# Optimization experiments

Hardware: AMD Instinct MI355X
Metric: run time of the kernel (lower is better)

Reference implementation:

```python
import jax, jax.numpy as jnp
import numpy as np


def _dct_ortho(x):
    # DCT-II with 'ortho' norm over the last axis, matching the torch impl.
    N = x.shape[-1]
    v = jnp.concatenate([x[..., ::2], x[..., 1::2][..., ::-1]], axis=-1)
    Vc = jnp.fft.fft(v, axis=-1)
    k = -jnp.arange(N, dtype=x.dtype) * (np.pi / (2 * N))
    V = Vc.real * jnp.cos(k) - Vc.imag * jnp.sin(k)
    scale = jnp.concatenate([
        jnp.full((1,), np.sqrt(N) * 2, dtype=x.dtype),
        jnp.full((N - 1,), np.sqrt(N / 2) * 2, dtype=x.dtype)])
    return 2 * (V / scale)


def _idct_ortho(X):
    # Inverse of _dct_ortho (DCT-III, 'ortho') over the last axis.
    N = X.shape[-1]
    Xv = X / 2
    scale = jnp.concatenate([
        jnp.full((1,), np.sqrt(N) * 2, dtype=X.dtype),
        jnp.full((N - 1,), np.sqrt(N / 2) * 2, dtype=X.dtype)])
    Xv = Xv * scale
    k = jnp.arange(N, dtype=X.dtype) * (np.pi / (2 * N))
    Wr, Wi = jnp.cos(k), jnp.sin(k)
    Vti = jnp.concatenate([jnp.zeros_like(Xv[..., :1]), -Xv[..., ::-1][..., :-1]], axis=-1)
    Vr = Xv * Wr - Vti * Wi
    Vi = Xv * Wi + Vti * Wr
    Vc = jax.lax.complex(Vr, Vi)
    # torch.fft.irfft(V, n=N) uses only the first N//2+1 complex entries.
    v = jnp.fft.irfft(Vc[..., : N // 2 + 1], n=N, axis=-1)
    out = jnp.zeros_like(v)
    out = out.at[..., ::2].set(v[..., : N - N // 2])
    out = out.at[..., 1::2].set(v[..., ::-1][..., : N // 2])
    return out


def _spectral_mix(xc, w):
    # xc: (B, I, A, B2, S) channel-first; w: (I, O, modes)
    modes = w.shape[-1]
    xf = _dct_ortho(xc)
    out = jnp.einsum('bixyz,ioz->boxyz', xf[..., :modes], w)
    out = jnp.pad(out, [(0, 0)] * 4 + [(0, xc.shape[-1] - modes)])
    return _idct_ortho(out)


def setup_inputs() -> dict:
    key = jax.random.key(0)
    ks = jax.random.split(key, 8)
    B, S, I, O, M = 4, 64, 32, 32, 16
    factor = 2
    x = jax.random.normal(ks[0], (B, S, S, S, I), dtype=jnp.float32)
    # xavier_normal_ for (in, out, modes): fan_in = out*modes, fan_out = in*modes
    std = float(np.sqrt(2.0 / (O * M + I * M)))
    fw_x = jax.random.normal(ks[1], (I, O, M), dtype=jnp.float32) * std
    fw_y = jax.random.normal(ks[2], (I, O, M), dtype=jnp.float32) * std
    fw_z = jax.random.normal(ks[3], (I, O, M), dtype=jnp.float32) * std
    # 2-layer backcast FF: Linear(O, O*factor) + ReLU, Linear(O*factor, O)
    lim0 = float(1.0 / np.sqrt(O))
    lim1 = float(1.0 / np.sqrt(O * factor))
    w0 = jax.random.uniform(ks[4], (O, O * factor), jnp.float32, -lim0, lim0)
    b0 = jax.random.uniform(ks[5], (O * factor,), jnp.float32, -lim0, lim0)
    w1 = jax.random.uniform(ks[6], (O * factor, O), jnp.float32, -lim1, lim1)
    b1 = jax.random.uniform(ks[7], (O,), jnp.float32, -lim1, lim1)
    return {"x": x, "fw_x": fw_x, "fw_y": fw_y, "fw_z": fw_z,
            "w0": w0, "b0": b0, "w1": w1, "b1": b1}


def reference(x, fw_x, fw_y, fw_z, w0, b0, w1, b1):
    # (B, S1, S2, S3, I) -> (B, I, S1, S2, S3)
    xc = jnp.transpose(x, (0, 4, 1, 2, 3))
    # z-axis (last dim already)
    xz = _spectral_mix(xc, fw_z)
    # y-axis
    xy = jnp.swapaxes(_spectral_mix(jnp.swapaxes(xc, -1, -2), fw_y), -1, -2)
    # x-axis
    xx = jnp.swapaxes(_spectral_mix(jnp.swapaxes(xc, -1, -3), fw_x), -1, -3)
    h = xx + xy + xz
    h = jnp.transpose(h, (0, 2, 3, 4, 1))  # back to channels-last
    # backcast FeedForward (dropout=0, eval): Linear -> ReLU -> Linear
    h = jax.nn.relu(h @ w0 + b0)
    b_out = h @ w1 + b1
    return b_out
```

## Files before the change

### kernel.cpp

```cpp
#include <hip/hip_runtime.h>
#include <math.h>

using f4 = __attribute__((ext_vector_type(4))) float;

#define NS 64
#define NI 32
#define NK 16

#define OFF_D   0
#define OFF_WTZ 1024
#define OFF_WTY (1024 + 16384)
#define OFF_WTX (1024 + 2*16384)
#define OFF_W0T (1024 + 3*16384)
#define WS_FLOATS (1024 + 3*16384 + 2048)

__device__ inline float dot4(f4 a, f4 b) { f4 p = a * b; return p[0] + p[1] + p[2] + p[3]; }

__global__ __launch_bounds__(256) void init_kernel(
    const float* __restrict__ fw_x, const float* __restrict__ fw_y,
    const float* __restrict__ fw_z, const float* __restrict__ w0,
    float* __restrict__ ws)
{
    int gid = blockIdx.x * 256 + threadIdx.x;
    if (gid < 1024) {
        int k = gid >> 6, n = gid & 63;
        float s = (k == 0) ? 0.125f : sqrtf(2.0f / 64.0f);
        ws[OFF_D + gid] = s * cospif((float)((2 * n + 1) * k) / 128.0f);
    } else if (gid < 1024 + 3 * 16384) {
        int r = gid - 1024;
        int a = r / 16384;
        int q = r % 16384;
        int k = q >> 10;
        int i = (q >> 5) & 31;
        int o = q & 31;
        const float* fw = (a == 0) ? fw_z : (a == 1) ? fw_y : fw_x;
        ws[1024 + a * 16384 + q] = fw[(i * 32 + o) * 16 + k];
    } else if (gid < WS_FLOATS) {
        int r = gid - (1024 + 3 * 16384);
        int j = r >> 5, i = r & 31;
        ws[OFF_W0T + r] = w0[i * 64 + j];
    }
}

template<int AXIS, int MODE>
__global__ __launch_bounds__(256) void axis_kernel(
    const float* __restrict__ x, float* __restrict__ h,
    const float* __restrict__ ws, const float* __restrict__ w1g,
    const float* __restrict__ b0g, const float* __restrict__ b1g)
{
    __shared__ f4 Xl[2048];
    __shared__ f4 Ul[512];
    __shared__ f4 Vl[512];
    __shared__ float Dl[1024];

    const int t = threadIdx.x;
    const int bid = blockIdx.x;
    const int b  = bid >> 10;
    const int c1 = (bid >> 4) & 63;
    const int c2 = bid & 15;

    const float* Dg = ws + OFF_D;
    const float* Wt = ws + (AXIS == 2 ? OFF_WTZ : AXIS == 1 ? OFF_WTY : OFF_WTX);

    int base, strideM, strideS;
    if (AXIS == 2) { base = ((b * 64 + c1) * 64 + c2 * 4) * 2048;      strideM = 32;     strideS = 2048; }
    if (AXIS == 1) { base = (b * 64 + c1) * 131072 + c2 * 128;         strideM = 2048;   strideS = 32; }
    if (AXIS == 0) { base = b * 8388608 + c1 * 2048 + c2 * 128;        strideM = 131072; strideS = 32; }

    #pragma unroll
    for (int q = 0; q < 4; ++q) Dl[t + 256 * q] = Dg[t + 256 * q];

    const f4* xg = reinterpret_cast<const f4*>(x);
    if (AXIS == 2) {
        int b4 = base >> 2;
        #pragma unroll
        for (int q = 0; q < 8; ++q) Xl[t + 256 * q] = xg[b4 + t + 256 * q];
    } else {
        #pragma unroll
        for (int q = 0; q < 8; ++q) {
            int j = t + 256 * q;
            int m = j >> 5, c = j & 31;
            Xl[j] = xg[((base + m * strideM) >> 2) + c];
        }
    }
    __syncthreads();

    #pragma unroll
    for (int it = 0; it < 2; ++it) {
        int id = t + 256 * it;
        int i4 = id & 7, k = (id >> 3) & 15, s = id >> 7;
        f4 acc = {0.f, 0.f, 0.f, 0.f};
        #pragma unroll
        for (int m = 0; m < 64; ++m) {
            f4 xv = Xl[AXIS == 2 ? (s * 512 + m * 8 + i4) : (m * 32 + s * 8 + i4)];
            acc += xv * Dl[k * 64 + m];
        }
        Ul[s * 128 + k * 8 + i4] = acc;
    }
    __syncthreads();

    if (t < 128) {
        int k = t >> 3, o4 = t & 7;
        const f4* Wt4 = reinterpret_cast<const f4*>(Wt);
        const float* Us = reinterpret_cast<const float*>(Ul);
        f4 v0 = {0.f,0.f,0.f,0.f}, v1 = v0, v2 = v0, v3 = v0;
        #pragma unroll 8
        for (int i = 0; i < 32; ++i) {
            f4 w = Wt4[k * 256 + i * 8 + o4];
            v0 += w * Us[0 * 512 + k * 32 + i];
            v1 += w * Us[1 * 512 + k * 32 + i];
            v2 += w * Us[2 * 512 + k * 32 + i];
            v3 += w * Us[3 * 512 + k * 32 + i];
        }
        Vl[0 * 128 + k * 8 + o4] = v0;
        Vl[1 * 128 + k * 8 + o4] = v1;
        Vl[2 * 128 + k * 8 + o4] = v2;
        Vl[3 * 128 + k * 8 + o4] = v3;
    }
    __syncthreads();

    f4* hg = reinterpret_cast<f4*>(h);
    #pragma unroll
    for (int it = 0; it < 8; ++it) {
        int id = t + 256 * it;
        int o4 = id & 7, n = (id >> 3) & 63, s = id >> 9;
        f4 acc = {0.f, 0.f, 0.f, 0.f};
        #pragma unroll
        for (int k = 0; k < 16; ++k)
            acc += Vl[s * 128 + k * 8 + o4] * Dl[k * 64 + n];
        int hi4 = ((base + n * strideM + s * strideS) >> 2) + o4;
        if constexpr (MODE == 2) {
            acc += hg[hi4];
            Xl[(s * 64 + n) * 8 + (o4 ^ (n & 7))] = acc;
        } else {
            if (MODE == 1) acc += hg[hi4];
            hg[hi4] = acc;
        }
    }

    if constexpr (MODE == 2) {
        __shared__ f4 w0s[512];
        __shared__ f4 w1s[512];
        __shared__ float b0s[64];
        __shared__ f4 b1s[8];
        const f4* w0t4 = reinterpret_cast<const f4*>(ws + OFF_W0T);
        const f4* w14  = reinterpret_cast<const f4*>(w1g);
        w0s[t] = w0t4[t];  w0s[t + 256] = w0t4[t + 256];
        w1s[t] = w14[t];   w1s[t + 256] = w14[t + 256];
        if (t < 64) b0s[t] = b0g[t];
        if (t < 8)  b1s[t] = reinterpret_cast<const f4*>(b1g)[t];
        __syncthreads();

        {
            int n = t & 63, sw = n & 7;
            f4 h0[8], a0[8];
            #pragma unroll
            for (int q = 0; q < 8; ++q) {
                h0[q] = Xl[t * 8 + (q ^ sw)];
                a0[q] = b1s[q];
            }
            #pragma unroll 8
            for (int j = 0; j < 64; ++j) {
                float s0 = b0s[j];
                #pragma unroll
                for (int q = 0; q < 8; ++q) s0 += dot4(h0[q], w0s[j * 8 + q]);
                s0 = fmaxf(s0, 0.f);
                #pragma unroll
                for (int q = 0; q < 8; ++q) a0[q] += w1s[j * 8 + q] * s0;
            }
            #pragma unroll
            for (int q = 0; q < 8; ++q) Xl[t * 8 + (q ^ sw)] = a0[q];
        }
        __syncthreads();

        #pragma unroll
        for (int it = 0; it < 8; ++it) {
            int id = t + 256 * it;
            int o4 = id & 7, n = (id >> 3) & 63, s = id >> 9;
            f4 v = Xl[(s * 64 + n) * 8 + (o4 ^ (n & 7))];
            hg[((base + n * strideM + s * strideS) >> 2) + o4] = v;
        }
    }
}

extern "C" void kernel_launch(void* const* d_in, const int* in_sizes, int n_in,
                              void* d_out, int out_size, void* d_ws, size_t ws_size,
                              hipStream_t stream)
{
    const float* x   = (const float*)d_in[0];
    const float* fwx = (const float*)d_in[1];
    const float* fwy = (const float*)d_in[2];
    const float* fwz = (const float*)d_in[3];
    const float* w0  = (const float*)d_in[4];
    const float* b0  = (const float*)d_in[5];
    const float* w1  = (const float*)d_in[6];
    const float* b1  = (const float*)d_in[7];
    float* out = (float*)d_out;
    float* ws  = (float*)d_ws;

    if (ws_size < WS_FLOATS * sizeof(float)) return;

    init_kernel<<<(WS_FLOATS + 255) / 256, 256, 0, stream>>>(fwx, fwy, fwz, w0, ws);
    axis_kernel<2, 0><<<4096, 256, 0, stream>>>(x, out, ws, w1, b0, b1);
    axis_kernel<1, 1><<<4096, 256, 0, stream>>>(x, out, ws, w1, b0, b1);
    axis_kernel<0, 2><<<4096, 256, 0, stream>>>(x, out, ws, w1, b0, b1);
}
```

Measured before the change: 746.0 us.

## Register-block DCT stages, pad and swizzle LDS, union shared buffers, restructure FFN

Each thread now computes several outputs per stage: two DCT modes in the forward transform and eight positions in the inverse. It reads D as padded f4 rows, which cuts LDS loads and bank conflicts. The spectral weight mix now uses all 256 threads instead of 128, with a rotated weight layout and a staggered i order to spread bank access. Ul/Vl and the FFN weight buffers share one LDS union, and launch_bounds requests 3 blocks per CU to raise occupancy. The FFN is reorganised into 16-wide hidden chunks using an untransposed w0. The main risk is higher register pressure.

```diff
diff --git a/kernel.cpp b/kernel.cpp
--- a/kernel.cpp
+++ b/kernel.cpp
@@ -3,55 +3,49 @@
 
 using f4 = __attribute__((ext_vector_type(4))) float;
 
-#define NS 64
-#define NI 32
-#define NK 16
-
 #define OFF_D   0
-#define OFF_WTZ 1024
-#define OFF_WTY (1024 + 16384)
-#define OFF_WTX (1024 + 2*16384)
-#define OFF_W0T (1024 + 3*16384)
-#define WS_FLOATS (1024 + 3*16384 + 2048)
-
-__device__ inline float dot4(f4 a, f4 b) { f4 p = a * b; return p[0] + p[1] + p[2] + p[3]; }
+#define OFF_WT  1024
+#define WS_FLOATS (1024 + 3*16384)
 
 __global__ __launch_bounds__(256) void init_kernel(
     const float* __restrict__ fw_x, const float* __restrict__ fw_y,
-    const float* __restrict__ fw_z, const float* __restrict__ w0,
-    float* __restrict__ ws)
+    const float* __restrict__ fw_z, float* __restrict__ ws)
 {
     int gid = blockIdx.x * 256 + threadIdx.x;
     if (gid < 1024) {
         int k = gid >> 6, n = gid & 63;
         float s = (k == 0) ? 0.125f : sqrtf(2.0f / 64.0f);
         ws[OFF_D + gid] = s * cospif((float)((2 * n + 1) * k) / 128.0f);
-    } else if (gid < 1024 + 3 * 16384) {
+    } else if (gid < WS_FLOATS) {
         int r = gid - 1024;
         int a = r / 16384;
         int q = r % 16384;
-        int k = q >> 10;
-        int i = (q >> 5) & 31;
-        int o = q & 31;
+        int k = q >> 10, i = (q >> 5) & 31, o = q & 31;
+        int o4 = o >> 2, ol = o & 3;
+        int o4r = (o4 + k) & 7;
         const float* fw = (a == 0) ? fw_z : (a == 1) ? fw_y : fw_x;
-        ws[1024 + a * 16384 + q] = fw[(i * 32 + o) * 16 + k];
-    } else if (gid < WS_FLOATS) {
-        int r = gid - (1024 + 3 * 16384);
-        int j = r >> 5, i = r & 31;
-        ws[OFF_W0T + r] = w0[i * 64 + j];
+        ws[OFF_WT + a * 16384 + k * 1024 + i * 32 + o4r * 4 + ol] = fw[(i * 32 + o) * 16 + k];
     }
 }
 
+union PhaseU {
+    struct { f4 Ul[512]; f4 Vl[512]; } p;
+    struct { f4 w0s[512]; f4 w1s[512]; } ff;
+};
+
 template<int AXIS, int MODE>
-__global__ __launch_bounds__(256) void axis_kernel(
+__global__ __launch_bounds__(256, 3) void axis_kernel(
     const float* __restrict__ x, float* __restrict__ h,
-    const float* __restrict__ ws, const float* __restrict__ w1g,
+    const float* __restrict__ ws,
+    const float* __restrict__ w0g, const float* __restrict__ w1g,
     const float* __restrict__ b0g, const float* __restrict__ b1g)
 {
     __shared__ f4 Xl[2048];
-    __shared__ f4 Ul[512];
-    __shared__ f4 Vl[512];
-    __shared__ float Dl[1024];
+    __shared__ PhaseU su;
+    __shared__ f4 Dl4[272];
+    __shared__ f4 b0sh[16];
+    __shared__ f4 b1sh[8];
+    float* Dl = reinterpret_cast<float*>(Dl4);
 
     const int t = threadIdx.x;
     const int bid = blockIdx.x;
@@ -60,15 +54,23 @@
     const int c2 = bid & 15;
 
     const float* Dg = ws + OFF_D;
-    const float* Wt = ws + (AXIS == 2 ? OFF_WTZ : AXIS == 1 ? OFF_WTY : OFF_WTX);
+    const float* Wt = ws + OFF_WT + (AXIS == 2 ? 0 : AXIS == 1 ? 16384 : 2 * 16384);
 
     int base, strideM, strideS;
-    if (AXIS == 2) { base = ((b * 64 + c1) * 64 + c2 * 4) * 2048;      strideM = 32;     strideS = 2048; }
-    if (AXIS == 1) { base = (b * 64 + c1) * 131072 + c2 * 128;         strideM = 2048;   strideS = 32; }
-    if (AXIS == 0) { base = b * 8388608 + c1 * 2048 + c2 * 128;        strideM = 131072; strideS = 32; }
+    if (AXIS == 2) { base = ((b * 64 + c1) * 64 + c2 * 4) * 2048; strideM = 32;     strideS = 2048; }
+    if (AXIS == 1) { base = (b * 64 + c1) * 131072 + c2 * 128;    strideM = 2048;   strideS = 32; }
+    if (AXIS == 0) { base = b * 8388608 + c1 * 2048 + c2 * 128;   strideM = 131072; strideS = 32; }
 
     #pragma unroll
-    for (int q = 0; q < 4; ++q) Dl[t + 256 * q] = Dg[t + 256 * q];
+    for (int q = 0; q < 4; ++q) {
+        int idx = t + 256 * q;
+        int k = idx >> 6, n = idx & 63;
+        Dl[k * 68 + n] = Dg[idx];
+    }
+    if constexpr (MODE == 2) {
+        if (t < 16) b0sh[t] = reinterpret_cast<const f4*>(b0g)[t];
+        else if (t < 24) b1sh[t - 16] = reinterpret_cast<const f4*>(b1g)[t - 16];
+    }
 
     const f4* xg = reinterpret_cast<const f4*>(x);
     if (AXIS == 2) {
@@ -85,98 +87,123 @@
     }
     __syncthreads();
 
-    #pragma unroll
-    for (int it = 0; it < 2; ++it) {
-        int id = t + 256 * it;
-        int i4 = id & 7, k = (id >> 3) & 15, s = id >> 7;
-        f4 acc = {0.f, 0.f, 0.f, 0.f};
-        #pragma unroll
-        for (int m = 0; m < 64; ++m) {
-            f4 xv = Xl[AXIS == 2 ? (s * 512 + m * 8 + i4) : (m * 32 + s * 8 + i4)];
-            acc += xv * Dl[k * 64 + m];
-        }
-        Ul[s * 128 + k * 8 + i4] = acc;
+    {
+        const int i4 = t & 7, kp = (t >> 3) & 7, s = t >> 6;
+        const int k0 = kp * 2;
+        f4 a0 = {0.f, 0.f, 0.f, 0.f}, a1 = a0;
+        #pragma unroll
+        for (int mq = 0; mq < 16; ++mq) {
+            f4 d0 = Dl4[k0 * 17 + mq];
+            f4 d1 = Dl4[(k0 + 1) * 17 + mq];
+            #pragma unroll
+            for (int e = 0; e < 4; ++e) {
+                int m = mq * 4 + e;
+                f4 xv = Xl[AXIS == 2 ? (s * 512 + m * 8 + i4) : (m * 32 + s * 8 + i4)];
+                a0 += xv * d0[e];
+                a1 += xv * d1[e];
+            }
+        }
+        su.p.Ul[s * 128 + k0 * 8 + i4] = a0;
+        su.p.Ul[s * 128 + (k0 + 1) * 8 + i4] = a1;
     }
     __syncthreads();
 
-    if (t < 128) {
-        int k = t >> 3, o4 = t & 7;
+    {
+        const int k = t >> 4, o4 = (t >> 1) & 7, sh = t & 1;
+        const int o4r = (o4 + k) & 7;
         const f4* Wt4 = reinterpret_cast<const f4*>(Wt);
-        const float* Us = reinterpret_cast<const float*>(Ul);
-        f4 v0 = {0.f,0.f,0.f,0.f}, v1 = v0, v2 = v0, v3 = v0;
-        #pragma unroll 8
-        for (int i = 0; i < 32; ++i) {
-            f4 w = Wt4[k * 256 + i * 8 + o4];
-            v0 += w * Us[0 * 512 + k * 32 + i];
-            v1 += w * Us[1 * 512 + k * 32 + i];
-            v2 += w * Us[2 * 512 + k * 32 + i];
-            v3 += w * Us[3 * 512 + k * 32 + i];
-        }
-        Vl[0 * 128 + k * 8 + o4] = v0;
-        Vl[1 * 128 + k * 8 + o4] = v1;
-        Vl[2 * 128 + k * 8 + o4] = v2;
-        Vl[3 * 128 + k * 8 + o4] = v3;
+        const float* Us = reinterpret_cast<const float*>(su.p.Ul);
+        f4 v0 = {0.f, 0.f, 0.f, 0.f}, v1 = v0;
+        #pragma unroll
+        for (int ii = 0; ii < 32; ++ii) {
+            int i = (ii + 4 * k) & 31;
+            f4 w = Wt4[k * 256 + i * 8 + o4r];
+            v0 += w * Us[(sh * 2) * 512 + k * 32 + i];
+            v1 += w * Us[(sh * 2 + 1) * 512 + k * 32 + i];
+        }
+        su.p.Vl[(sh * 2) * 128 + k * 8 + o4] = v0;
+        su.p.Vl[(sh * 2 + 1) * 128 + k * 8 + o4] = v1;
     }
     __syncthreads();
 
     f4* hg = reinterpret_cast<f4*>(h);
-    #pragma unroll
-    for (int it = 0; it < 8; ++it) {
-        int id = t + 256 * it;
-        int o4 = id & 7, n = (id >> 3) & 63, s = id >> 9;
-        f4 acc = {0.f, 0.f, 0.f, 0.f};
-        #pragma unroll
-        for (int k = 0; k < 16; ++k)
-            acc += Vl[s * 128 + k * 8 + o4] * Dl[k * 64 + n];
-        int hi4 = ((base + n * strideM + s * strideS) >> 2) + o4;
-        if constexpr (MODE == 2) {
-            acc += hg[hi4];
-            Xl[(s * 64 + n) * 8 + (o4 ^ (n & 7))] = acc;
-        } else {
-            if (MODE == 1) acc += hg[hi4];
-            hg[hi4] = acc;
+    const int o4 = t & 7, nc = (t >> 3) & 7, s = t >> 6;
+    {
+        const int n0 = nc * 8;
+        f4 acc[8];
+        #pragma unroll
+        for (int j = 0; j < 8; ++j) acc[j] = f4{0.f, 0.f, 0.f, 0.f};
+        #pragma unroll
+        for (int k = 0; k < 16; ++k) {
+            f4 v  = su.p.Vl[s * 128 + k * 8 + o4];
+            f4 d0 = Dl4[k * 17 + nc * 2];
+            f4 d1 = Dl4[k * 17 + nc * 2 + 1];
+            acc[0] += v * d0[0]; acc[1] += v * d0[1];
+            acc[2] += v * d0[2]; acc[3] += v * d0[3];
+            acc[4] += v * d1[0]; acc[5] += v * d1[1];
+            acc[6] += v * d1[2]; acc[7] += v * d1[3];
+        }
+        #pragma unroll
+        for (int j = 0; j < 8; ++j) {
+            int n = n0 + j;
+            int hi4 = ((base + n * strideM + s * strideS) >> 2) + o4;
+            if constexpr (MODE == 0) {
+                hg[hi4] = acc[j];
+            } else if constexpr (MODE == 1) {
+                hg[hi4] = acc[j] + hg[hi4];
+            } else {
+                Xl[(s * 64 + n) * 8 + (o4 ^ (n & 7))] = acc[j] + hg[hi4];
+            }
         }
     }
 
     if constexpr (MODE == 2) {
-        __shared__ f4 w0s[512];
-        __shared__ f4 w1s[512];
-        __shared__ float b0s[64];
-        __shared__ f4 b1s[8];
-        const f4* w0t4 = reinterpret_cast<const f4*>(ws + OFF_W0T);
-        const f4* w14  = reinterpret_cast<const f4*>(w1g);
-        w0s[t] = w0t4[t];  w0s[t + 256] = w0t4[t + 256];
-        w1s[t] = w14[t];   w1s[t + 256] = w14[t + 256];
-        if (t < 64) b0s[t] = b0g[t];
-        if (t < 8)  b1s[t] = reinterpret_cast<const f4*>(b1g)[t];
         __syncthreads();
-
-        {
-            int n = t & 63, sw = n & 7;
-            f4 h0[8], a0[8];
+        const f4* w0g4 = reinterpret_cast<const f4*>(w0g);
+        const f4* w1g4 = reinterpret_cast<const f4*>(w1g);
+        su.ff.w0s[t] = w0g4[t];  su.ff.w0s[t + 256] = w0g4[t + 256];
+        su.ff.w1s[t] = w1g4[t];  su.ff.w1s[t + 256] = w1g4[t + 256];
+        __syncthreads();
+
+        const int sw = t & 7;
+        f4 h0[8], out[8];
+        #pragma unroll
+        for (int q = 0; q < 8; ++q) {
+            h0[q]  = Xl[t * 8 + (q ^ sw)];
+            out[q] = b1sh[q];
+        }
+        #pragma unroll 1
+        for (int jc = 0; jc < 4; ++jc) {
+            f4 z0 = b0sh[jc * 4 + 0], z1 = b0sh[jc * 4 + 1];
+            f4 z2 = b0sh[jc * 4 + 2], z3 = b0sh[jc * 4 + 3];
             #pragma unroll
-            for (int q = 0; q < 8; ++q) {
-                h0[q] = Xl[t * 8 + (q ^ sw)];
-                a0[q] = b1s[q];
-            }
-            #pragma unroll 8
-            for (int j = 0; j < 64; ++j) {
-                float s0 = b0s[j];
+            for (int i = 0; i < 32; ++i) {
+                float hi = h0[i >> 2][i & 3];
+                z0 += su.ff.w0s[i * 16 + jc * 4 + 0] * hi;
+                z1 += su.ff.w0s[i * 16 + jc * 4 + 1] * hi;
+                z2 += su.ff.w0s[i * 16 + jc * 4 + 2] * hi;
+                z3 += su.ff.w0s[i * 16 + jc * 4 + 3] * hi;
+            }
+            #pragma unroll
+            for (int u = 0; u < 4; ++u) {
+                f4 zu = (u == 0) ? z0 : (u == 1) ? z1 : (u == 2) ? z2 : z3;
                 #pragma unroll
-                for (int q = 0; q < 8; ++q) s0 += dot4(h0[q], w0s[j * 8 + q]);
-                s0 = fmaxf(s0, 0.f);
-                #pragma unroll
-                for (int q = 0; q < 8; ++q) a0[q] += w1s[j * 8 + q] * s0;
-            }
-            #pragma unroll
-            for (int q = 0; q < 8; ++q) Xl[t * 8 + (q ^ sw)] = a0[q];
-        }
+                for (int e = 0; e < 4; ++e) {
+                    float zz = fmaxf(zu[e], 0.f);
+                    int j = jc * 16 + u * 4 + e;
+                    #pragma unroll
+                    for (int q = 0; q < 8; ++q)
+                        out[q] += su.ff.w1s[j * 8 + q] * zz;
+                }
+            }
+        }
+        #pragma unroll
+        for (int q = 0; q < 8; ++q) Xl[t * 8 + (q ^ sw)] = out[q];
         __syncthreads();
 
         #pragma unroll
-        for (int it = 0; it < 8; ++it) {
-            int id = t + 256 * it;
-            int o4 = id & 7, n = (id >> 3) & 63, s = id >> 9;
+        for (int j = 0; j < 8; ++j) {
+            int n = nc * 8 + j;
             f4 v = Xl[(s * 64 + n) * 8 + (o4 ^ (n & 7))];
             hg[((base + n * strideM + s * strideS) >> 2) + o4] = v;
         }
@@ -200,8 +227,8 @@
 
     if (ws_size < WS_FLOATS * sizeof(float)) return;
 
-    init_kernel<<<(WS_FLOATS + 255) / 256, 256, 0, stream>>>(fwx, fwy, fwz, w0, ws);
-    axis_kernel<2, 0><<<4096, 256, 0, stream>>>(x, out, ws, w1, b0, b1);
-    axis_kernel<1, 1><<<4096, 256, 0, stream>>>(x, out, ws, w1, b0, b1);
-    axis_kernel<0, 2><<<4096, 256, 0, stream>>>(x, out, ws, w1, b0, b1);
+    init_kernel<<<(WS_FLOATS + 255) / 256, 256, 0, stream>>>(fwx, fwy, fwz, ws);
+    axis_kernel<2, 0><<<4096, 256, 0, stream>>>(x, out, ws, w0, w1, b0, b1);
+    axis_kernel<1, 1><<<4096, 256, 0, stream>>>(x, out, ws, w0, w1, b0, b1);
+    axis_kernel<0, 2><<<4096, 256, 0, stream>>>(x, out, ws, w0, w1, b0, b1);
 }
```

Result: slower. 1.104 ms (+48.0%).
